# Kernel tuning notes

Measured on AMD Instinct MI355X. Metric: run time of the kernel, lower is better.

The kernel has to match this reference:

```python
import jax, jax.numpy as jnp
import numpy as np

FRAMES = 4
SLICE = 14
BATCH = 4
NODES = 2 * FRAMES * SLICE * SLICE  # 1568
C = 2048
LN_EPS = 1e-5


def _layer(x, w, g, b):
    # Linear(no bias) -> LayerNorm(2048) -> LeakyReLU(0.1)
    y = jnp.einsum('bnc,dc->bnd', x, w)
    m = jnp.mean(y, axis=-1, keepdims=True)
    v = jnp.mean((y - m) ** 2, axis=-1, keepdims=True)
    y = (y - m) / jnp.sqrt(v + LN_EPS) * g + b
    return jax.nn.leaky_relu(y, 0.1)


def setup_inputs() -> dict:
    key = jax.random.key(0)
    ks = jax.random.split(key, 8)
    w = lambda k, sh: (jax.random.normal(k, sh, jnp.float32) * 0.02)
    return {
        'x': jax.random.normal(ks[0], (BATCH, NODES, C), jnp.float32),
        'w_fc1': w(ks[1], (C, C)),
        'w1': w(ks[2], (C, C)), 'g1': jnp.ones((C,), jnp.float32), 'b1': jnp.zeros((C,), jnp.float32),
        'w2': w(ks[3], (C, C)), 'g2': jnp.ones((C,), jnp.float32), 'b2': jnp.zeros((C,), jnp.float32),
        'w3': w(ks[4], (C, C)), 'g3': jnp.ones((C,), jnp.float32), 'b3': jnp.zeros((C,), jnp.float32),
        'conv1_w': w(ks[5], (2 * FRAMES,)),            # Conv2d(2F->1, k=1) weight squeezed
        'conv1_b': jnp.zeros((1,), jnp.float32),
        'deconv_w': w(ks[6], (C, 1024, 3, 3)),          # ConvTranspose2d weight [in, out, kH, kW]
        'deconv_b': jnp.zeros((1024,), jnp.float32),
    }


def reference(x, w_fc1, w1, g1, b1, w2, g2, b2, w3, g3, b3, conv1_w, conv1_b, deconv_w, deconv_b):
    # ---- adjacency_laplacian ----
    h = jnp.einsum('bnc,dc->bnd', x, w_fc1)                 # fc1
    s = jnp.einsum('bnd,bmd->bnm', h, h)                    # out @ out^T
    sq = s * s
    adj = sq / jnp.sum(sq, axis=1, keepdims=True)           # square_normalize (sum over dim=1)
    adj = adj + jnp.eye(NODES, dtype=adj.dtype)             # A + I
    d = 1.0 / jnp.sqrt(jnp.sum(adj, axis=1))                # [B, n]
    # D^{-1/2} A D^{-1/2}: diag matmuls are exactly row/col scaling
    lap = d[:, :, None] * adj * d[:, None, :]

    # ---- graph-conv stack ----
    out = jnp.matmul(lap, x)
    out = _layer(out, w1, g1, b1)
    out = jnp.matmul(lap, out)
    out = _layer(out, w2, g2, b2)
    out = jnp.matmul(lap, out)
    out = _layer(out, w3, g3, b3)

    # ---- head: transpose, reshape, 1x1 conv over 2F frame-channels ----
    out = jnp.swapaxes(out, 1, 2)                           # [B, 2048, nodes]
    out = out.reshape(BATCH * C, 2 * FRAMES, SLICE, SLICE)
    out = jnp.einsum('nfhw,f->nhw', out, conv1_w) + conv1_b[0]
    out = out.reshape(BATCH, C, SLICE, SLICE)

    # bilinear upsample x2 (align_corners=False == half-pixel, matches jax.image.resize)
    out = jax.image.resize(out, (BATCH, C, 2 * SLICE, 2 * SLICE), method='bilinear')

    # ConvTranspose2d(2048->1024, k=3, pad=1, stride=3) as dilated conv with flipped kernel
    wk = jnp.flip(deconv_w, axis=(-2, -1)).transpose(1, 0, 2, 3)  # [out, in, 3, 3]
    out = jax.lax.conv_general_dilated(
        out, wk, window_strides=(1, 1), padding=((1, 1), (1, 1)),
        lhs_dilation=(3, 3), dimension_numbers=('NCHW', 'OIHW', 'NCHW'))
    out = out + deconv_b[None, :, None, None]               # [B, 1024, 82, 82]
    return out
```

## Files before the change

kernel.cpp:

```cpp
#include <hip/hip_runtime.h>

typedef __bf16 bf16;
typedef __bf16 bf16x4 __attribute__((ext_vector_type(4)));
typedef __bf16 bf16x8 __attribute__((ext_vector_type(8)));
typedef float f32x4 __attribute__((ext_vector_type(4)));

#define N_NODES 1568
#define CDIM 2048

__device__ __forceinline__ void async_copy16(const bf16* g, bf16* l) {
    __builtin_amdgcn_global_load_lds(
        (const __attribute__((address_space(1))) unsigned int*)g,
        (__attribute__((address_space(3))) unsigned int*)l, 16, 0, 0);
}

template <typename OUT_T>
__global__ __launch_bounds__(256, 2) void gemm_nt(const bf16* __restrict__ A,
                                                  const bf16* __restrict__ B,
                                                  OUT_T* __restrict__ C,
                                                  int M, int N, int K,
                                                  long sAb, long sBb, long sCb) {
    __shared__ __align__(16) bf16 sA[128 * 32];
    __shared__ __align__(16) bf16 sB[128 * 32];
    const int bz = blockIdx.z;
    A += (long)bz * sAb; B += (long)bz * sBb; C += (long)bz * sCb;
    const int m0 = blockIdx.x * 128, n0 = blockIdx.y * 128;
    const int t = threadIdx.x;
    const int lane = t & 63, wave = t >> 6;
    const int wr = wave >> 1, wc = wave & 1;
    const int l15 = lane & 15, quad = lane >> 4;

    f32x4 acc[4][4];
#pragma unroll
    for (int i = 0; i < 4; i++)
#pragma unroll
        for (int j = 0; j < 4; j++) acc[i][j] = (f32x4){0.f, 0.f, 0.f, 0.f};

    const int ko = (t & 3) * 8;
    int ra1 = m0 + (t >> 2);          if (ra1 >= M) ra1 = M - 1;
    int ra2 = m0 + ((t + 256) >> 2);  if (ra2 >= M) ra2 = M - 1;
    int rb1 = n0 + (t >> 2);          if (rb1 >= N) rb1 = N - 1;
    int rb2 = n0 + ((t + 256) >> 2);  if (rb2 >= N) rb2 = N - 1;
    const bf16* gA1 = A + (long)ra1 * K + ko;
    const bf16* gA2 = A + (long)ra2 * K + ko;
    const bf16* gB1 = B + (long)rb1 * K + ko;
    const bf16* gB2 = B + (long)rb2 * K + ko;
    bf16* lA1 = sA + t * 8;  bf16* lA2 = sA + (t + 256) * 8;
    bf16* lB1 = sB + t * 8;  bf16* lB2 = sB + (t + 256) * 8;

    for (int k0 = 0; k0 < K; k0 += 32) {
        __syncthreads();
        async_copy16(gA1 + k0, lA1);
        async_copy16(gA2 + k0, lA2);
        async_copy16(gB1 + k0, lB1);
        async_copy16(gB2 + k0, lB2);
        __syncthreads();
        bf16x8 af[4], bfr[4];
#pragma unroll
        for (int i = 0; i < 4; i++)
            af[i] = *(const bf16x8*)(sA + (wr * 64 + i * 16 + l15) * 32 + quad * 8);
#pragma unroll
        for (int j = 0; j < 4; j++)
            bfr[j] = *(const bf16x8*)(sB + (wc * 64 + j * 16 + l15) * 32 + quad * 8);
#pragma unroll
        for (int i = 0; i < 4; i++)
#pragma unroll
            for (int j = 0; j < 4; j++)
                acc[i][j] = __builtin_amdgcn_mfma_f32_16x16x32_bf16(af[i], bfr[j], acc[i][j], 0, 0, 0);
    }
#pragma unroll
    for (int i = 0; i < 4; i++) {
        const int row0 = m0 + wr * 64 + i * 16 + quad * 4;
#pragma unroll
        for (int j = 0; j < 4; j++) {
            const int col = n0 + wc * 64 + j * 16 + l15;
            if (col < N) {
#pragma unroll
                for (int r = 0; r < 4; r++) {
                    const int row = row0 + r;
                    if (row < M) C[(long)row * N + col] = (OUT_T)acc[i][j][r];
                }
            }
        }
    }
}

__global__ __launch_bounds__(256, 2) void gemm_nt_sym(const bf16* __restrict__ A,
                                                      float* __restrict__ C,
                                                      int M, int K,
                                                      long sAb, long sCb) {
    __shared__ __align__(16) bf16 sA[128 * 32];
    __shared__ __align__(16) bf16 sB[128 * 32];
    const int bz = blockIdx.z;
    A += (long)bz * sAb; C += (long)bz * sCb;
    int rem = blockIdx.x, bi = 0;
    while (rem >= 13 - bi) { rem -= 13 - bi; bi++; }
    const int bj = bi + rem;
    const int m0 = bi * 128, n0 = bj * 128;
    const int t = threadIdx.x;
    const int lane = t & 63, wave = t >> 6;
    const int wr = wave >> 1, wc = wave & 1;
    const int l15 = lane & 15, quad = lane >> 4;

    f32x4 acc[4][4];
#pragma unroll
    for (int i = 0; i < 4; i++)
#pragma unroll
        for (int j = 0; j < 4; j++) acc[i][j] = (f32x4){0.f, 0.f, 0.f, 0.f};

    const int ko = (t & 3) * 8;
    int ra1 = m0 + (t >> 2);          if (ra1 >= M) ra1 = M - 1;
    int ra2 = m0 + ((t + 256) >> 2);  if (ra2 >= M) ra2 = M - 1;
    int rb1 = n0 + (t >> 2);          if (rb1 >= M) rb1 = M - 1;
    int rb2 = n0 + ((t + 256) >> 2);  if (rb2 >= M) rb2 = M - 1;
    const bf16* gA1 = A + (long)ra1 * K + ko;
    const bf16* gA2 = A + (long)ra2 * K + ko;
    const bf16* gB1 = A + (long)rb1 * K + ko;
    const bf16* gB2 = A + (long)rb2 * K + ko;
    bf16* lA1 = sA + t * 8;  bf16* lA2 = sA + (t + 256) * 8;
    bf16* lB1 = sB + t * 8;  bf16* lB2 = sB + (t + 256) * 8;

    for (int k0 = 0; k0 < K; k0 += 32) {
        __syncthreads();
        async_copy16(gA1 + k0, lA1);
        async_copy16(gA2 + k0, lA2);
        async_copy16(gB1 + k0, lB1);
        async_copy16(gB2 + k0, lB2);
        __syncthreads();
        bf16x8 af[4], bfr[4];
#pragma unroll
        for (int i = 0; i < 4; i++)
            af[i] = *(const bf16x8*)(sA + (wr * 64 + i * 16 + l15) * 32 + quad * 8);
#pragma unroll
        for (int j = 0; j < 4; j++)
            bfr[j] = *(const bf16x8*)(sB + (wc * 64 + j * 16 + l15) * 32 + quad * 8);
#pragma unroll
        for (int i = 0; i < 4; i++)
#pragma unroll
            for (int j = 0; j < 4; j++)
                acc[i][j] = __builtin_amdgcn_mfma_f32_16x16x32_bf16(af[i], bfr[j], acc[i][j], 0, 0, 0);
    }
    const bool mirror = (bi != bj);
#pragma unroll
    for (int i = 0; i < 4; i++) {
        const int row0 = m0 + wr * 64 + i * 16 + quad * 4;
#pragma unroll
        for (int j = 0; j < 4; j++) {
            const int col = n0 + wc * 64 + j * 16 + l15;
            if (col < M) {
#pragma unroll
                for (int r = 0; r < 4; r++) {
                    const int row = row0 + r;
                    if (row < M) {
                        const float v = acc[i][j][r];
                        C[(long)row * M + col] = v;
                        if (mirror) C[(long)col * M + row] = v;
                    }
                }
            }
        }
    }
}

__global__ __launch_bounds__(256) void cast_f32_bf16_k(const float* __restrict__ in,
                                                       bf16* __restrict__ out, long n) {
    long i = ((long)blockIdx.x * 256 + threadIdx.x) * 4;
    if (i >= n) return;
    float4 v = *(const float4*)(in + i);
    bf16x4 o;
    o[0] = (bf16)v.x; o[1] = (bf16)v.y; o[2] = (bf16)v.z; o[3] = (bf16)v.w;
    *(bf16x4*)(out + i) = o;
}

__global__ __launch_bounds__(256) void cast4_f32_bf16_k(const float* __restrict__ a,
                                                        const float* __restrict__ b,
                                                        const float* __restrict__ c,
                                                        const float* __restrict__ d,
                                                        bf16* __restrict__ out, long n) {
    const int w = blockIdx.y;
    const float* in = (w == 0) ? a : (w == 1) ? b : (w == 2) ? c : d;
    bf16* o = out + (long)w * n;
    long i = ((long)blockIdx.x * 256 + threadIdx.x) * 4;
    if (i >= n) return;
    float4 v = *(const float4*)(in + i);
    bf16x4 ov;
    ov[0] = (bf16)v.x; ov[1] = (bf16)v.y; ov[2] = (bf16)v.z; ov[3] = (bf16)v.w;
    *(bf16x4*)(o + i) = ov;
}

__global__ __launch_bounds__(256) void transpose_bf16_k(const bf16* __restrict__ in,
                                                        bf16* __restrict__ out,
                                                        int R, int C, long sIn, long sOut) {
    __shared__ bf16 tile[64][65];
    in += (long)blockIdx.z * sIn;
    out += (long)blockIdx.z * sOut;
    const int r0 = blockIdx.y * 64, c0 = blockIdx.x * 64;
    const int tx = threadIdx.x & 63, ty = threadIdx.x >> 6;
#pragma unroll
    for (int i = 0; i < 16; i++) {
        int r = ty * 16 + i;
        int gr = r0 + r, gc = c0 + tx;
        tile[r][tx] = (gr < R && gc < C) ? in[(long)gr * C + gc] : (bf16)0.f;
    }
    __syncthreads();
#pragma unroll
    for (int i = 0; i < 16; i++) {
        int c = ty * 16 + i;
        int gc = c0 + c, gr = r0 + tx;
        if (gc < C && gr < R) out[(long)gc * R + gr] = tile[tx][c];
    }
}

__global__ __launch_bounds__(256) void colsum_part_k(const float* __restrict__ s,
                                                     float* __restrict__ part) {
    int m = blockIdx.x * 256 + threadIdx.x;
    if (m >= N_NODES) return;
    int y = blockIdx.y, b = blockIdx.z;
    const float* sb = s + (long)b * N_NODES * N_NODES;
    float acc = 0.f;
    for (int n = y * 196; n < y * 196 + 196; ++n) {
        float v = sb[(long)n * N_NODES + m];
        acc += v * v;
    }
    part[((long)y * 4 + b) * N_NODES + m] = acc;
}

__global__ __launch_bounds__(256) void colsum_comb_k(const float* __restrict__ part,
                                                     float* __restrict__ inv) {
    int m = blockIdx.x * 256 + threadIdx.x;
    if (m >= N_NODES) return;
    int b = blockIdx.y;
    float a = 0.f;
#pragma unroll
    for (int y = 0; y < 8; y++) a += part[((long)y * 4 + b) * N_NODES + m];
    inv[(long)b * N_NODES + m] = 1.0f / a;
}

__global__ __launch_bounds__(256) void lap_build_k(const float* __restrict__ s,
                                                   const float* __restrict__ inv,
                                                   bf16* __restrict__ lap) {
    int m = blockIdx.x * 256 + threadIdx.x;
    if (m >= N_NODES) return;
    int n = blockIdx.y, b = blockIdx.z;
    long off = (long)b * N_NODES * N_NODES + (long)n * N_NODES + m;
    float v = s[off];
    float l = 0.5f * v * v * inv[(long)b * N_NODES + m];
    if (n == m) l += 0.5f;
    lap[off] = (bf16)l;
}

__global__ __launch_bounds__(256) void ln_leaky_k(const float* __restrict__ y,
                                                  const float* __restrict__ g,
                                                  const float* __restrict__ beta,
                                                  bf16* __restrict__ z) {
    const long row = blockIdx.x;
    const float* yr = y + row * CDIM;
    const int t = threadIdx.x;
    float v[8];
    float s = 0.f, ss = 0.f;
#pragma unroll
    for (int i = 0; i < 8; i++) {
        float x = yr[t + 256 * i];
        v[i] = x; s += x; ss += x * x;
    }
#pragma unroll
    for (int o = 32; o > 0; o >>= 1) {
        s += __shfl_down(s, o);
        ss += __shfl_down(ss, o);
    }
    __shared__ float sh[8];
    const int wave = t >> 6;
    if ((t & 63) == 0) { sh[wave] = s; sh[wave + 4] = ss; }
    __syncthreads();
    if (t == 0) {
        float a = 0.f, b2 = 0.f;
#pragma unroll
        for (int w = 0; w < 4; w++) { a += sh[w]; b2 += sh[w + 4]; }
        sh[0] = a; sh[4] = b2;
    }
    __syncthreads();
    const float mean = sh[0] * (1.f / 2048.f);
    const float var = sh[4] * (1.f / 2048.f) - mean * mean;
    const float invs = rsqrtf(var + 1e-5f);
    bf16* zr = z + row * CDIM;
#pragma unroll
    for (int i = 0; i < 8; i++) {
        int c = t + 256 * i;
        float o = (v[i] - mean) * invs * g[c] + beta[c];
        o = o > 0.f ? o : 0.1f * o;
        zr[c] = (bf16)o;
    }
}

__global__ __launch_bounds__(256) void conv1_k(const bf16* __restrict__ z,
                                               const float* __restrict__ cw,
                                               const float* __restrict__ cb,
                                               bf16* __restrict__ tb) {
    const int b = blockIdx.z, hw = blockIdx.y;
    const int c = blockIdx.x * 256 + threadIdx.x;
    float acc = cb[0];
#pragma unroll
    for (int f = 0; f < 8; f++)
        acc += (float)z[((long)b * N_NODES + f * 196 + hw) * CDIM + c] * cw[f];
    tb[((long)b * 196 + hw) * CDIM + c] = (bf16)acc;
}

__global__ __launch_bounds__(256) void upsample_k(const bf16* __restrict__ tb,
                                                  bf16* __restrict__ u) {
    const int b = blockIdx.z, i = blockIdx.y, j = blockIdx.x;
    const float si = 0.5f * i - 0.25f, sj = 0.5f * j - 0.25f;
    const int i0 = (int)floorf(si), j0 = (int)floorf(sj);
    const float wi = si - i0, wj = sj - j0;
    const int i0c = max(i0, 0), i1c = min(i0 + 1, 13);
    const int j0c = max(j0, 0), j1c = min(j0 + 1, 13);
    const bf16* base = tb + (long)b * 196 * CDIM;
    const long r00 = ((long)i0c * 14 + j0c) * CDIM, r01 = ((long)i0c * 14 + j1c) * CDIM;
    const long r10 = ((long)i1c * 14 + j0c) * CDIM, r11 = ((long)i1c * 14 + j1c) * CDIM;
    bf16* ur = u + ((long)(b * 28 + i) * 28 + j) * CDIM;
    const float w00 = (1.f - wi) * (1.f - wj), w01 = (1.f - wi) * wj;
    const float w10 = wi * (1.f - wj), w11 = wi * wj;
    for (int k = 0; k < 8; k++) {
        int cc = threadIdx.x + 256 * k;
        float v = w00 * (float)base[r00 + cc] + w01 * (float)base[r01 + cc] +
                  w10 * (float)base[r10 + cc] + w11 * (float)base[r11 + cc];
        ur[cc] = (bf16)v;
    }
}

__global__ __launch_bounds__(256) void wt_k(const float* __restrict__ dw,
                                            bf16* __restrict__ Wt) {
    const int ic = blockIdx.x * 256 + threadIdx.x;
    const int oc = blockIdx.y;
    const float* src = dw + ((long)ic * 1024 + oc) * 9;
#pragma unroll
    for (int r = 0; r < 3; r++)
#pragma unroll
        for (int s = 0; s < 3; s++) {
            int kh = 2 - r, kw = 2 - s;
            Wt[((long)(kh * 3 + kw) * 1024 + oc) * 2048 + ic] = (bf16)src[r * 3 + s];
        }
}

__global__ __launch_bounds__(256) void deconv_scatter_k(const bf16* __restrict__ r,
                                                        const float* __restrict__ db,
                                                        float* __restrict__ out) {
    const int blk = blockIdx.x;
    const int b = blk >> 10, oc = blk & 1023;
    const float bias = db[oc];
    float* ob = out + (long)blk * 82 * 82;
    for (int e = threadIdx.x; e < 82 * 82; e += 256) {
        const int oh = e / 82, ow = e - oh * 82;
        const int mh = oh % 3, mw = ow % 3;
        const int kh = (mh == 0) ? 1 : ((mh == 1) ? 0 : 2);
        const int kw = (mw == 0) ? 1 : ((mw == 1) ? 0 : 2);
        const int ih = (oh - (1 - kh)) / 3;
        const int iw = (ow - (1 - kw)) / 3;
        const int g = kh * 3 + kw;
        ob[e] = (float)r[(long)(g * 1024 + oc) * 3136 + b * 784 + ih * 28 + iw] + bias;
    }
}

extern "C" void kernel_launch(void* const* d_in, const int* in_sizes, int n_in,
                              void* d_out, int out_size, void* d_ws, size_t ws_size,
                              hipStream_t stream) {
    const float* x        = (const float*)d_in[0];
    const float* w_fc1    = (const float*)d_in[1];
    const float* w1       = (const float*)d_in[2];
    const float* g1       = (const float*)d_in[3];
    const float* b1       = (const float*)d_in[4];
    const float* w2       = (const float*)d_in[5];
    const float* g2       = (const float*)d_in[6];
    const float* b2       = (const float*)d_in[7];
    const float* w3       = (const float*)d_in[8];
    const float* g3       = (const float*)d_in[9];
    const float* b3       = (const float*)d_in[10];
    const float* conv1_w  = (const float*)d_in[11];
    const float* conv1_b  = (const float*)d_in[12];
    const float* deconv_w = (const float*)d_in[13];
    const float* deconv_b = (const float*)d_in[14];
    float* out = (float*)d_out;

    char* W = (char*)d_ws;
    bf16* wb   = (bf16*)(W + 0);
    bf16* xb   = (bf16*)(W + 33554432);
    bf16* xbT  = (bf16*)(W + 59244544);
    bf16* hb   = (bf16*)(W + 84934656);
    bf16* lap  = (bf16*)(W + 110624768);
    bf16* tbuf = (bf16*)(W + 130293760);
    bf16* ubuf = (bf16*)(W + 133505024);
    bf16* Wt   = (bf16*)(W + 146350080);
    float* ybuf = (float*)(W + 184098816);
    float* sbuf = (float*)(W + 184098816);
    float* part = (float*)(W + 235479040);
    float* invc = (float*)(W + 235679744);
    bf16* rbuf = (bf16*)(W + 0);
    bf16* zb = xb;
    bf16* zT = xbT;
    bf16* outN = hb;

    const long WMAT = (long)2048 * 2048;
    bf16* wb0 = wb, *wb1 = wb + WMAT, *wb2 = wb + 2 * WMAT, *wb3 = wb + 3 * WMAT;

    cast4_f32_bf16_k<<<dim3(4096, 4), 256, 0, stream>>>(w_fc1, w1, w2, w3, wb, WMAT);
    cast_f32_bf16_k<<<dim3(12544), 256, 0, stream>>>(x, xb, (long)6272 * 2048);
    wt_k<<<dim3(8, 1024), 256, 0, stream>>>(deconv_w, Wt);

    transpose_bf16_k<<<dim3(32, 25, 4), 256, 0, stream>>>(
        xb, xbT, N_NODES, CDIM, (long)N_NODES * CDIM, (long)N_NODES * CDIM);

    gemm_nt<bf16><<<dim3(49, 16, 1), 256, 0, stream>>>(
        xb, wb0, hb, 6272, 2048, 2048, 0, 0, 0);

    gemm_nt_sym<<<dim3(91, 1, 4), 256, 0, stream>>>(
        hb, sbuf, N_NODES, 2048,
        (long)N_NODES * 2048, (long)N_NODES * N_NODES);

    colsum_part_k<<<dim3(7, 8, 4), 256, 0, stream>>>(sbuf, part);
    colsum_comb_k<<<dim3(7, 4), 256, 0, stream>>>(part, invc);
    lap_build_k<<<dim3(7, N_NODES, 4), 256, 0, stream>>>(sbuf, invc, lap);

    const bf16* wlayer[3] = {wb1, wb2, wb3};
    const float* gl[3] = {g1, g2, g3};
    const float* bl[3] = {b1, b2, b3};
    for (int i = 0; i < 3; i++) {
        const bf16* prevT = (i == 0) ? xbT : zT;
        gemm_nt<bf16><<<dim3(13, 16, 4), 256, 0, stream>>>(
            lap, prevT, outN, N_NODES, CDIM, N_NODES,
            (long)N_NODES * N_NODES, (long)CDIM * N_NODES, (long)N_NODES * CDIM);
        gemm_nt<float><<<dim3(49, 16, 1), 256, 0, stream>>>(
            outN, wlayer[i], ybuf, 6272, 2048, 2048, 0, 0, 0);
        ln_leaky_k<<<dim3(6272), 256, 0, stream>>>(ybuf, gl[i], bl[i], zb);
        if (i < 2) {
            transpose_bf16_k<<<dim3(32, 25, 4), 256, 0, stream>>>(
                zb, zT, N_NODES, CDIM, (long)N_NODES * CDIM, (long)N_NODES * CDIM);
        }
    }

    conv1_k<<<dim3(8, 196, 4), 256, 0, stream>>>(zb, conv1_w, conv1_b, tbuf);
    upsample_k<<<dim3(28, 28, 4), 256, 0, stream>>>(tbuf, ubuf);
    gemm_nt<bf16><<<dim3(72, 25, 1), 256, 0, stream>>>(
        Wt, ubuf, rbuf, 9216, 3136, 2048, 0, 0, 0);
    deconv_scatter_k<<<dim3(4096), 256, 0, stream>>>(rbuf, deconv_b, out);

    (void)in_sizes; (void)n_in; (void)out_size; (void)ws_size;
}
```

Measured before the change: 1.256 ms.

## Add 256x256-tile double-buffered GEMM for the large dense matmuls

Introduces a 512-thread GEMM kernel with 256x256 output tiles, 64-wide K steps, XOR-swizzled LDS, async global-to-LDS double buffering, and interleaved LDS reads with MFMA issue under raised priority. It replaces the 128x128 GEMM for the fc1 projection, the three per-layer weight projections, and the deconvolution GEMM. The aim is more data reuse per LDS load and overlap of global loads with compute. In exchange it uses 128KB of LDS and many registers per block, and it has fewer blocks (200 for the 6272x2048 shapes), which can leave CUs underfilled or imbalanced on a large-CU part.

```diff
diff --git a/kernel.cpp b/kernel.cpp
--- a/kernel.cpp
+++ b/kernel.cpp
@@ -12,6 +12,119 @@
     __builtin_amdgcn_global_load_lds(
         (const __attribute__((address_space(1))) unsigned int*)g,
         (__attribute__((address_space(3))) unsigned int*)l, 16, 0, 0);
+}
+
+template <typename OUT_T>
+__global__ __launch_bounds__(512, 2) void gemm256_nt(const bf16* __restrict__ A,
+                                                     const bf16* __restrict__ B,
+                                                     OUT_T* __restrict__ C,
+                                                     int M, int N, int K) {
+    __shared__ __align__(16) bf16 lds[2][2][256 * 64];
+    const int m0 = blockIdx.x * 256, n0 = blockIdx.y * 256;
+    const int t = threadIdx.x;
+    const int lane = t & 63, wave = t >> 6;
+    const int wm = wave >> 2, wn = wave & 3;
+    const int l15 = lane & 15, quad = lane >> 4, rx7 = l15 & 7;
+
+    const int cg = (((t & 7) ^ ((t >> 3) & 7)) << 3);
+    const int rb = t >> 3;
+    const bf16* ga[4];
+    const bf16* gb[4];
+#pragma unroll
+    for (int i = 0; i < 4; i++) {
+        int ra = m0 + rb + i * 64; if (ra >= M) ra = M - 1;
+        int rn = n0 + rb + i * 64; if (rn >= N) rn = N - 1;
+        ga[i] = A + (long)ra * K + cg;
+        gb[i] = B + (long)rn * K + cg;
+    }
+    const int ldst = t * 8;
+
+    f32x4 acc[8][4];
+#pragma unroll
+    for (int i = 0; i < 8; i++)
+#pragma unroll
+        for (int j = 0; j < 4; j++) acc[i][j] = (f32x4){0.f, 0.f, 0.f, 0.f};
+
+    auto stage = [&](int buf, int k0) {
+        bf16* sAx = &lds[buf][0][0];
+        bf16* sBx = &lds[buf][1][0];
+#pragma unroll
+        for (int i = 0; i < 4; i++)
+            async_copy16(ga[i] + k0, sAx + ldst + i * 4096);
+#pragma unroll
+        for (int i = 0; i < 4; i++)
+            async_copy16(gb[i] + k0, sBx + ldst + i * 4096);
+    };
+
+    const int NT = K >> 6;
+    stage(0, 0);
+    stage(1, 64);
+    asm volatile("s_waitcnt vmcnt(8)" ::: "memory");
+    __builtin_amdgcn_s_barrier();
+
+    bf16x8 bfr[4][2], afr[2][2];
+    for (int tt = 0; tt < NT; ++tt) {
+        const bf16* sA = &lds[tt & 1][0][0];
+        const bf16* sB = &lds[tt & 1][1][0];
+
+        auto rdB = [&]() {
+#pragma unroll
+            for (int nf = 0; nf < 4; ++nf)
+#pragma unroll
+                for (int kk = 0; kk < 2; ++kk)
+                    bfr[nf][kk] = *(const bf16x8*)(sB + (wn * 64 + nf * 16 + l15) * 64 +
+                                                   ((((kk << 2) | quad) ^ rx7) << 3));
+        };
+        auto rdA = [&](int q) {
+#pragma unroll
+            for (int mi = 0; mi < 2; ++mi)
+#pragma unroll
+                for (int kk = 0; kk < 2; ++kk)
+                    afr[mi][kk] = *(const bf16x8*)(sA + (wm * 128 + (q * 2 + mi) * 16 + l15) * 64 +
+                                                   ((((kk << 2) | quad) ^ rx7) << 3));
+        };
+        auto mfq = [&](int q) {
+            __builtin_amdgcn_s_setprio(1);
+#pragma unroll
+            for (int kk = 0; kk < 2; ++kk)
+#pragma unroll
+                for (int mi = 0; mi < 2; ++mi)
+#pragma unroll
+                    for (int nf = 0; nf < 4; ++nf)
+                        acc[q * 2 + mi][nf] = __builtin_amdgcn_mfma_f32_16x16x32_bf16(
+                            afr[mi][kk], bfr[nf][kk], acc[q * 2 + mi][nf], 0, 0, 0);
+            __builtin_amdgcn_s_setprio(0);
+        };
+
+        rdB();
+        rdA(0); mfq(0);
+        rdA(1); mfq(1);
+        rdA(2); mfq(2);
+        rdA(3);
+        asm volatile("s_waitcnt lgkmcnt(0)" ::: "memory");
+        __builtin_amdgcn_s_barrier();
+        if (tt + 2 < NT) stage(tt & 1, (tt + 2) << 6);
+        mfq(3);
+        if (tt + 2 < NT) { asm volatile("s_waitcnt vmcnt(8)" ::: "memory"); }
+        else             { asm volatile("s_waitcnt vmcnt(0)" ::: "memory"); }
+        __builtin_amdgcn_s_barrier();
+    }
+
+#pragma unroll
+    for (int mf = 0; mf < 8; ++mf) {
+        const int row0 = m0 + wm * 128 + mf * 16 + quad * 4;
+#pragma unroll
+        for (int nf = 0; nf < 4; ++nf) {
+            const int col = n0 + wn * 64 + nf * 16 + l15;
+            if (col < N) {
+#pragma unroll
+                for (int r = 0; r < 4; ++r) {
+                    const int row = row0 + r;
+                    if (row < M) C[(long)row * N + col] = (OUT_T)acc[mf][nf][r];
+                }
+            }
+        }
+    }
 }
 
 template <typename OUT_T>
@@ -408,8 +521,7 @@
     transpose_bf16_k<<<dim3(32, 25, 4), 256, 0, stream>>>(
         xb, xbT, N_NODES, CDIM, (long)N_NODES * CDIM, (long)N_NODES * CDIM);
 
-    gemm_nt<bf16><<<dim3(49, 16, 1), 256, 0, stream>>>(
-        xb, wb0, hb, 6272, 2048, 2048, 0, 0, 0);
+    gemm256_nt<bf16><<<dim3(25, 8), 512, 0, stream>>>(xb, wb0, hb, 6272, 2048, 2048);
 
     gemm_nt_sym<<<dim3(91, 1, 4), 256, 0, stream>>>(
         hb, sbuf, N_NODES, 2048,
@@ -427,8 +539,8 @@
         gemm_nt<bf16><<<dim3(13, 16, 4), 256, 0, stream>>>(
             lap, prevT, outN, N_NODES, CDIM, N_NODES,
             (long)N_NODES * N_NODES, (long)CDIM * N_NODES, (long)N_NODES * CDIM);
-        gemm_nt<float><<<dim3(49, 16, 1), 256, 0, stream>>>(
-            outN, wlayer[i], ybuf, 6272, 2048, 2048, 0, 0, 0);
+        gemm256_nt<float><<<dim3(25, 8), 512, 0, stream>>>(
+            outN, wlayer[i], ybuf, 6272, 2048, 2048);
         ln_leaky_k<<<dim3(6272), 256, 0, stream>>>(ybuf, gl[i], bl[i], zb);
         if (i < 2) {
             transpose_bf16_k<<<dim3(32, 25, 4), 256, 0, stream>>>(
@@ -438,8 +550,7 @@
 
     conv1_k<<<dim3(8, 196, 4), 256, 0, stream>>>(zb, conv1_w, conv1_b, tbuf);
     upsample_k<<<dim3(28, 28, 4), 256, 0, stream>>>(tbuf, ubuf);
-    gemm_nt<bf16><<<dim3(72, 25, 1), 256, 0, stream>>>(
-        Wt, ubuf, rbuf, 9216, 3136, 2048, 0, 0, 0);
+    gemm256_nt<bf16><<<dim3(36, 13), 512, 0, stream>>>(Wt, ubuf, rbuf, 9216, 3136, 2048);
     deconv_scatter_k<<<dim3(4096), 256, 0, stream>>>(rbuf, deconv_b, out);
 
     (void)in_sizes; (void)n_in; (void)out_size; (void)ws_size;
```

New measurement: 1.177 ms. 1.07x faster.
